# Optimization experiments

Measured on AMD Instinct MI355X. Metric: run time of the kernel, lower is better.

## Reference

```python
import jax, jax.numpy as jnp
import numpy as np

B, TQ, TS, E, D = 8, 100, 100, 512, 512

def setup_inputs() -> dict:
    key = jax.random.key(0)
    k1, k2, k3, k4, k5 = jax.random.split(key, 5)
    src_reps = jax.random.normal(k1, (B, TQ, TS, E), dtype=jnp.float32)
    tgt_reps = jax.random.normal(k2, (B, TQ, TS, E), dtype=jnp.float32)
    mask = jnp.ones((B, TQ, TS), dtype=jnp.float32)
    # attn_1: Linear(2E -> D) with bias; attn_2: Linear(D -> 1) no bias
    W1 = jax.random.normal(k3, (2 * E, D), dtype=jnp.float32) / np.sqrt(2 * E)
    b1 = jax.random.normal(k4, (D,), dtype=jnp.float32) * 0.01
    w2 = jax.random.normal(k5, (D,), dtype=jnp.float32) / np.sqrt(D)
    return {"src_reps": src_reps, "tgt_reps": tgt_reps, "mask": mask,
            "W1": W1, "b1": b1, "w2": w2}

def reference(src_reps, tgt_reps, mask, W1, b1, w2):
    # cat over feature dim: [B,TQ,TS,2E]
    cat_reps = jnp.concatenate([src_reps, tgt_reps], axis=-1)
    # two small linears + tanh -> scores [B,TQ,TS]
    h = jnp.tanh(jnp.einsum('bqse,ed->bqsd', cat_reps, W1) + b1)
    attn_scores = jnp.einsum('bqsd,d->bqs', h, w2)
    attn_scores = mask * attn_scores  # multiplicative mask (as in source)
    attn_weights = jax.nn.softmax(attn_scores, axis=2)
    # weighted sum over src dim -> [B,TQ,E]
    attn_out = jnp.einsum('bqs,bqse->bqe', attn_weights, src_reps)
    return (attn_out, attn_weights)
```

## Files before the change

kernel.cpp:

```cpp
#include <hip/hip_runtime.h>
#include <hip/hip_bf16.h>

#define B_   8
#define TQ_  100
#define TS_  100
#define E_   512
#define D_   512
#define K_   1024
#define M_   (B_*TQ_*TS_)

#define MT   128
#define NT   512
#define BK   64
#define NTHREADS 512

typedef __attribute__((ext_vector_type(4))) float f32x4;
typedef __attribute__((ext_vector_type(8))) short bf16x8;

__device__ __forceinline__ short f2bf(float f) {
  __hip_bfloat16 h = __float2bfloat16(f);
  return *reinterpret_cast<short*>(&h);
}

__device__ __forceinline__ float fast_tanh(float x) {
  float e = __expf(2.0f * x);
  return 1.0f - 2.0f / (e + 1.0f);
}

__device__ __forceinline__ void gld16(const void* g, void* l) {
  __builtin_amdgcn_global_load_lds(
      (const __attribute__((address_space(1))) unsigned int*)g,
      (__attribute__((address_space(3))) unsigned int*)l, 16, 0, 0);
}

__global__ void prep_w1(const float* __restrict__ W1, short* __restrict__ W1sw) {
  int idx = blockIdx.x * 256 + threadIdx.x;
  int k = idx >> 9;
  int n = idx & (D_ - 1);
  int byte = (k * 2) ^ ((n & 7) << 4);
  W1sw[(size_t)n * K_ + (byte >> 1)] = f2bf(W1[idx]);
}

__launch_bounds__(NTHREADS, 2)
__global__ void scores_kernel(const float* __restrict__ src,
                              const float* __restrict__ tgt,
                              const short* __restrict__ W1sw,
                              const float* __restrict__ b1,
                              const float* __restrict__ w2,
                              float* __restrict__ scores) {
  __shared__ __align__(16) char Alds[2][MT * 128];
  __shared__ __align__(16) char Blds[2][NT * 128];

  const int tid  = threadIdx.x;
  const int wave = tid >> 6;
  const int lane = tid & 63;
  const int lr   = lane & 15;
  const int lg   = lane >> 4;
  const int wr   = wave >> 2;
  const int wc   = wave & 3;
  const int m0   = blockIdx.x * MT;

  f32x4 acc[4][8];
  #pragma unroll
  for (int i = 0; i < 4; i++)
    #pragma unroll
    for (int j = 0; j < 8; j++)
      acc[i][j] = (f32x4){0.f, 0.f, 0.f, 0.f};

  const int ra  = tid >> 2;
  const int ka  = (tid & 3) * 16;
  const int swA = (ra & 7) << 4;
  const int br = tid >> 3;
  const int bb = (tid & 7) * 16;

  #define ISSUE_A(R0,R1,R2,R3,K0)                                              \
    {                                                                          \
      const float* Ap = (((K0) < E_) ? src : tgt)                              \
                        + (size_t)(m0 + ra) * E_ + ((K0) & (E_ - 1)) + ka;     \
      R0 = *reinterpret_cast<const f32x4*>(Ap);                                \
      R1 = *reinterpret_cast<const f32x4*>(Ap + 4);                            \
      R2 = *reinterpret_cast<const f32x4*>(Ap + 8);                            \
      R3 = *reinterpret_cast<const f32x4*>(Ap + 12);                           \
    }

  #define WRITE_A(R0,R1,R2,R3,BUF)                                             \
    {                                                                          \
      bf16x8 w0, w1;                                                           \
      w0[0]=f2bf(R0[0]); w0[1]=f2bf(R0[1]); w0[2]=f2bf(R0[2]); w0[3]=f2bf(R0[3]);\
      w0[4]=f2bf(R1[0]); w0[5]=f2bf(R1[1]); w0[6]=f2bf(R1[2]); w0[7]=f2bf(R1[3]);\
      w1[0]=f2bf(R2[0]); w1[1]=f2bf(R2[1]); w1[2]=f2bf(R2[2]); w1[3]=f2bf(R2[3]);\
      w1[4]=f2bf(R3[0]); w1[5]=f2bf(R3[1]); w1[6]=f2bf(R3[2]); w1[7]=f2bf(R3[3]);\
      int kb = ka * 2;                                                         \
      *reinterpret_cast<bf16x8*>((BUF) + ra * 128 + ( kb       ^ swA)) = w0;   \
      *reinterpret_cast<bf16x8*>((BUF) + ra * 128 + ((kb + 16) ^ swA)) = w1;   \
    }

  #define ISSUE_B(K0,BUF)                                                      \
    {                                                                          \
      _Pragma("unroll")                                                        \
      for (int j = 0; j < 8; j++) {                                            \
        const char* gp = (const char*)W1sw + (size_t)(j * 64 + br) * 2048      \
                         + (size_t)(K0) * 2 + bb;                              \
        gld16(gp, (BUF) + j * 8192 + tid * 16);                                \
      }                                                                        \
    }

  #define MFMA_PHASE(KK,AB,BB2)                                                \
    {                                                                          \
      const int kb = (KK) * 64 + lg * 16;                                      \
      bf16x8 a[4], b[8];                                                       \
      _Pragma("unroll")                                                        \
      for (int mi = 0; mi < 4; mi++) {                                         \
        int row = wr * 64 + mi * 16 + lr;                                      \
        a[mi] = *reinterpret_cast<const bf16x8*>(                              \
                    (AB) + row * 128 + (kb ^ ((row & 7) << 4)));               \
      }                                                                        \
      _Pragma("unroll")                                                        \
      for (int ni = 0; ni < 8; ni++) {                                         \
        int nr = wc * 128 + ni * 16 + lr;                                      \
        b[ni] = *reinterpret_cast<const bf16x8*>(                              \
                    (BB2) + nr * 128 + (kb ^ ((nr & 7) << 4)));                \
      }                                                                        \
      __builtin_amdgcn_s_setprio(1);                                           \
      _Pragma("unroll")                                                        \
      for (int mi = 0; mi < 4; mi++)                                           \
        _Pragma("unroll")                                                      \
        for (int ni = 0; ni < 8; ni++)                                         \
          acc[mi][ni] = __builtin_amdgcn_mfma_f32_16x16x32_bf16(               \
                            a[mi], b[ni], acc[mi][ni], 0, 0, 0);               \
      __builtin_amdgcn_s_setprio(0);                                           \
    }

  {
    f32x4 r0, r1, r2, r3;
    ISSUE_A(r0, r1, r2, r3, 0);
    ISSUE_B(0, Blds[0]);
    WRITE_A(r0, r1, r2, r3, Alds[0]);
  }
  __syncthreads();

  for (int t = 0; t < 16; ++t) {
    const int cur = t & 1;
    const int nxt = cur ^ 1;
    const bool pf = (t < 15);
    const int k0n = (t + 1) * BK;
    f32x4 r0, r1, r2, r3;
    if (pf) ISSUE_A(r0, r1, r2, r3, k0n);
    MFMA_PHASE(0, Alds[cur], Blds[cur]);
    if (pf) {
      ISSUE_B(k0n, Blds[nxt]);
      WRITE_A(r0, r1, r2, r3, Alds[nxt]);
    }
    MFMA_PHASE(1, Alds[cur], Blds[cur]);
    __syncthreads();
  }

  float* s_sc = (float*)Alds;
  if (tid < MT) s_sc[tid] = 0.0f;
  __syncthreads();

  float b1v[8], w2v[8];
  #pragma unroll
  for (int ni = 0; ni < 8; ni++) {
    int n = wc * 128 + ni * 16 + lr;
    b1v[ni] = b1[n];
    w2v[ni] = w2[n];
  }
  #pragma unroll
  for (int mi = 0; mi < 4; mi++) {
    #pragma unroll
    for (int r = 0; r < 4; r++) {
      float p = 0.0f;
      #pragma unroll
      for (int ni = 0; ni < 8; ni++)
        p += fast_tanh(acc[mi][ni][r] + b1v[ni]) * w2v[ni];
      p += __shfl_xor(p, 1);
      p += __shfl_xor(p, 2);
      p += __shfl_xor(p, 4);
      p += __shfl_xor(p, 8);
      if (lr == 0) atomicAdd(&s_sc[wr * 64 + mi * 16 + lg * 4 + r], p);
    }
  }
  __syncthreads();
  if (tid < MT) scores[m0 + tid] = s_sc[tid];
}

__global__ void softmax_wsum(const float* __restrict__ src,
                             const float* __restrict__ mask,
                             const float* __restrict__ scores,
                             float* __restrict__ out) {
  const int row = blockIdx.x;
  const int tid = threadIdx.x;
  __shared__ float s_e[TS_];

  float v = 0.0f;
  if (tid < TS_) {
    v = scores[row * TS_ + tid] * mask[row * TS_ + tid];
    s_e[tid] = v;
  }
  __syncthreads();
  float mx = -3.0e38f;
  for (int s = 0; s < TS_; s++) mx = fmaxf(mx, s_e[s]);
  __syncthreads();
  if (tid < TS_) s_e[tid] = __expf(v - mx);
  __syncthreads();
  float sum = 0.0f;
  for (int s = 0; s < TS_; s++) sum += s_e[s];
  const float inv = 1.0f / sum;

  float* out_attn = out;
  float* out_w    = out + (size_t)B_ * TQ_ * E_;
  if (tid < TS_) out_w[row * TS_ + tid] = s_e[tid] * inv;

  const float* sp = src + (size_t)row * TS_ * E_ + tid;
  float acc = 0.0f;
  #pragma unroll 4
  for (int s = 0; s < TS_; s++) acc = fmaf(s_e[s], sp[(size_t)s * E_], acc);
  out_attn[row * E_ + tid] = acc * inv;
}

extern "C" void kernel_launch(void* const* d_in, const int* in_sizes, int n_in,
                              void* d_out, int out_size, void* d_ws, size_t ws_size,
                              hipStream_t stream) {
  const float* src  = (const float*)d_in[0];
  const float* tgt  = (const float*)d_in[1];
  const float* mask = (const float*)d_in[2];
  const float* W1   = (const float*)d_in[3];
  const float* b1   = (const float*)d_in[4];
  const float* w2   = (const float*)d_in[5];

  short* W1sw   = (short*)d_ws;
  float* scores = (float*)((char*)d_ws + (size_t)D_ * K_ * 2);

  float* out = (float*)d_out;

  hipLaunchKernelGGL(prep_w1, dim3((K_ * D_) / 256), dim3(256), 0, stream, W1, W1sw);
  hipLaunchKernelGGL(scores_kernel, dim3(M_ / MT), dim3(NTHREADS), 0, stream,
                     src, tgt, W1sw, b1, w2, scores);
  hipLaunchKernelGGL(softmax_wsum, dim3(B_ * TQ_), dim3(512), 0, stream,
                     src, mask, scores, out);
}
```

Baseline: 187.2 us.

## Interleave GEMM K-loop into four barrier-separated phases with explicit waitcnts

Restructures the scores GEMM main loop into four sub-phases, each reading two B column tiles from LDS and issuing a slice of the next tile's global loads (A fp32 loads, B global_load_lds in halves, then the A bf16 write). Raw s_barrier and explicit s_waitcnt with sched_barrier replace __syncthreads, so memory traffic is spread between MFMA bursts instead of clustered. A fragments for both k halves are loaded once per tile. The cost is more barriers per iteration and fragile hand-tuned vmcnt counts.

```diff
diff --git a/kernel.cpp b/kernel.cpp
--- a/kernel.cpp
+++ b/kernel.cpp
@@ -9,8 +9,7 @@
 #define K_   1024
 #define M_   (B_*TQ_*TS_)
 
-#define MT   128
-#define NT   512
+#define BM   128
 #define BK   64
 #define NTHREADS 512
 
@@ -48,8 +47,8 @@
                               const float* __restrict__ b1,
                               const float* __restrict__ w2,
                               float* __restrict__ scores) {
-  __shared__ __align__(16) char Alds[2][MT * 128];
-  __shared__ __align__(16) char Blds[2][NT * 128];
+  __shared__ __align__(16) char Alds[2][BM * 128];
+  __shared__ __align__(16) char Blds[2][D_ * 128];
 
   const int tid  = threadIdx.x;
   const int wave = tid >> 6;
@@ -58,7 +57,7 @@
   const int lg   = lane >> 4;
   const int wr   = wave >> 2;
   const int wc   = wave & 3;
-  const int m0   = blockIdx.x * MT;
+  const int m0   = blockIdx.x * BM;
 
   f32x4 acc[4][8];
   #pragma unroll
@@ -68,95 +67,141 @@
       acc[i][j] = (f32x4){0.f, 0.f, 0.f, 0.f};
 
   const int ra  = tid >> 2;
-  const int ka  = (tid & 3) * 16;
-  const int swA = (ra & 7) << 4;
-  const int br = tid >> 3;
-  const int bb = (tid & 7) * 16;
-
-  #define ISSUE_A(R0,R1,R2,R3,K0)                                              \
-    {                                                                          \
-      const float* Ap = (((K0) < E_) ? src : tgt)                              \
-                        + (size_t)(m0 + ra) * E_ + ((K0) & (E_ - 1)) + ka;     \
-      R0 = *reinterpret_cast<const f32x4*>(Ap);                                \
-      R1 = *reinterpret_cast<const f32x4*>(Ap + 4);                            \
-      R2 = *reinterpret_cast<const f32x4*>(Ap + 8);                            \
-      R3 = *reinterpret_cast<const f32x4*>(Ap + 12);                           \
-    }
-
-  #define WRITE_A(R0,R1,R2,R3,BUF)                                             \
-    {                                                                          \
-      bf16x8 w0, w1;                                                           \
-      w0[0]=f2bf(R0[0]); w0[1]=f2bf(R0[1]); w0[2]=f2bf(R0[2]); w0[3]=f2bf(R0[3]);\
-      w0[4]=f2bf(R1[0]); w0[5]=f2bf(R1[1]); w0[6]=f2bf(R1[2]); w0[7]=f2bf(R1[3]);\
-      w1[0]=f2bf(R2[0]); w1[1]=f2bf(R2[1]); w1[2]=f2bf(R2[2]); w1[3]=f2bf(R2[3]);\
-      w1[4]=f2bf(R3[0]); w1[5]=f2bf(R3[1]); w1[6]=f2bf(R3[2]); w1[7]=f2bf(R3[3]);\
-      int kb = ka * 2;                                                         \
-      *reinterpret_cast<bf16x8*>((BUF) + ra * 128 + ( kb       ^ swA)) = w0;   \
-      *reinterpret_cast<bf16x8*>((BUF) + ra * 128 + ((kb + 16) ^ swA)) = w1;   \
-    }
-
-  #define ISSUE_B(K0,BUF)                                                      \
-    {                                                                          \
+  const int kaf = (tid & 3) * 16;
+  const int asw = (ra & 7) << 4;
+  const size_t arow = (size_t)(m0 + ra) * E_;
+  const size_t bgrow = (size_t)(tid >> 3) * 2048 + (size_t)(tid & 7) * 16;
+
+  #define WAIT_LGKM0  { asm volatile("s_waitcnt lgkmcnt(0)" ::: "memory"); \
+                        __builtin_amdgcn_sched_barrier(0); }
+  #define BAR         __builtin_amdgcn_s_barrier()
+
+  #define RD_B(BB, NI0, CUR)                                                   \
+    _Pragma("unroll")                                                          \
+    for (int u = 0; u < 2; u++) {                                              \
+      int n = wc * 128 + ((NI0) + u) * 16 + lr;                                \
       _Pragma("unroll")                                                        \
-      for (int j = 0; j < 8; j++) {                                            \
-        const char* gp = (const char*)W1sw + (size_t)(j * 64 + br) * 2048      \
-                         + (size_t)(K0) * 2 + bb;                              \
-        gld16(gp, (BUF) + j * 8192 + tid * 16);                                \
-      }                                                                        \
-    }
-
-  #define MFMA_PHASE(KK,AB,BB2)                                                \
-    {                                                                          \
-      const int kb = (KK) * 64 + lg * 16;                                      \
-      bf16x8 a[4], b[8];                                                       \
+      for (int kk = 0; kk < 2; kk++)                                           \
+        BB[u][kk] = *(const bf16x8*)(Blds[CUR] + n * 128 +                     \
+                        ((kk * 64 + lg * 16) ^ ((n & 7) << 4)));               \
+    }
+
+  #define MFMA8(BB, NI0)                                                       \
+    { __builtin_amdgcn_s_setprio(1);                                           \
       _Pragma("unroll")                                                        \
-      for (int mi = 0; mi < 4; mi++) {                                         \
-        int row = wr * 64 + mi * 16 + lr;                                      \
-        a[mi] = *reinterpret_cast<const bf16x8*>(                              \
-                    (AB) + row * 128 + (kb ^ ((row & 7) << 4)));               \
-      }                                                                        \
-      _Pragma("unroll")                                                        \
-      for (int ni = 0; ni < 8; ni++) {                                         \
-        int nr = wc * 128 + ni * 16 + lr;                                      \
-        b[ni] = *reinterpret_cast<const bf16x8*>(                              \
-                    (BB2) + nr * 128 + (kb ^ ((nr & 7) << 4)));                \
-      }                                                                        \
-      __builtin_amdgcn_s_setprio(1);                                           \
-      _Pragma("unroll")                                                        \
-      for (int mi = 0; mi < 4; mi++)                                           \
+      for (int kk = 0; kk < 2; kk++)                                           \
         _Pragma("unroll")                                                      \
-        for (int ni = 0; ni < 8; ni++)                                         \
-          acc[mi][ni] = __builtin_amdgcn_mfma_f32_16x16x32_bf16(               \
-                            a[mi], b[ni], acc[mi][ni], 0, 0, 0);               \
-      __builtin_amdgcn_s_setprio(0);                                           \
-    }
+        for (int mi = 0; mi < 4; mi++)                                         \
+          _Pragma("unroll")                                                    \
+          for (int u = 0; u < 2; u++)                                          \
+            acc[mi][(NI0) + u] = __builtin_amdgcn_mfma_f32_16x16x32_bf16(      \
+                a[mi][kk], BB[u][kk], acc[mi][(NI0) + u], 0, 0, 0);            \
+      __builtin_amdgcn_s_setprio(0); }
 
   {
-    f32x4 r0, r1, r2, r3;
-    ISSUE_A(r0, r1, r2, r3, 0);
-    ISSUE_B(0, Blds[0]);
-    WRITE_A(r0, r1, r2, r3, Alds[0]);
-  }
-  __syncthreads();
+    #pragma unroll
+    for (int j = 0; j < 8; j++)
+      gld16((const char*)W1sw + (size_t)j * 131072 + bgrow,
+            Blds[0] + j * 8192 + wave * 1024);
+    const float* Ap = src + arow + kaf;
+    f32x4 r0 = *(const f32x4*)(Ap);
+    f32x4 r1 = *(const f32x4*)(Ap + 4);
+    f32x4 r2 = *(const f32x4*)(Ap + 8);
+    f32x4 r3 = *(const f32x4*)(Ap + 12);
+    bf16x8 w0, w1;
+    w0[0]=f2bf(r0[0]); w0[1]=f2bf(r0[1]); w0[2]=f2bf(r0[2]); w0[3]=f2bf(r0[3]);
+    w0[4]=f2bf(r1[0]); w0[5]=f2bf(r1[1]); w0[6]=f2bf(r1[2]); w0[7]=f2bf(r1[3]);
+    w1[0]=f2bf(r2[0]); w1[1]=f2bf(r2[1]); w1[2]=f2bf(r2[2]); w1[3]=f2bf(r2[3]);
+    w1[4]=f2bf(r3[0]); w1[5]=f2bf(r3[1]); w1[6]=f2bf(r3[2]); w1[7]=f2bf(r3[3]);
+    int kb = kaf * 2;
+    *(bf16x8*)(Alds[0] + ra * 128 + ( kb       ^ asw)) = w0;
+    *(bf16x8*)(Alds[0] + ra * 128 + ((kb + 16) ^ asw)) = w1;
+    asm volatile("s_waitcnt vmcnt(0) lgkmcnt(0)" ::: "memory");
+    __builtin_amdgcn_sched_barrier(0);
+    BAR;
+  }
 
   for (int t = 0; t < 16; ++t) {
     const int cur = t & 1;
     const int nxt = cur ^ 1;
     const bool pf = (t < 15);
-    const int k0n = (t + 1) * BK;
+    const int kn  = (t + 1) * BK;
     f32x4 r0, r1, r2, r3;
-    if (pf) ISSUE_A(r0, r1, r2, r3, k0n);
-    MFMA_PHASE(0, Alds[cur], Blds[cur]);
-    if (pf) {
-      ISSUE_B(k0n, Blds[nxt]);
-      WRITE_A(r0, r1, r2, r3, Alds[nxt]);
-    }
-    MFMA_PHASE(1, Alds[cur], Blds[cur]);
-    __syncthreads();
+    bf16x8 a[4][2];
+
+    #pragma unroll
+    for (int mi = 0; mi < 4; mi++) {
+      int row = wr * 64 + mi * 16 + lr;
+      #pragma unroll
+      for (int kk = 0; kk < 2; kk++)
+        a[mi][kk] = *(const bf16x8*)(Alds[cur] + row * 128 +
+                        ((kk * 64 + lg * 16) ^ ((row & 7) << 4)));
+    }
+    {
+      bf16x8 bb[2][2];
+      RD_B(bb, 0, cur);
+      if (pf) {
+        const float* Ap = ((kn < E_) ? src : tgt) + arow + (kn & (E_ - 1)) + kaf;
+        r0 = *(const f32x4*)(Ap);
+        r1 = *(const f32x4*)(Ap + 4);
+        r2 = *(const f32x4*)(Ap + 8);
+        r3 = *(const f32x4*)(Ap + 12);
+      }
+      BAR; WAIT_LGKM0;
+      MFMA8(bb, 0);
+      BAR;
+    }
+    {
+      bf16x8 bb[2][2];
+      RD_B(bb, 2, cur);
+      if (pf) {
+        #pragma unroll
+        for (int j = 0; j < 4; j++)
+          gld16((const char*)W1sw + (size_t)j * 131072 + (size_t)kn * 2 + bgrow,
+                Blds[nxt] + j * 8192 + wave * 1024);
+      }
+      BAR; WAIT_LGKM0;
+      MFMA8(bb, 2);
+      BAR;
+    }
+    {
+      bf16x8 bb[2][2];
+      RD_B(bb, 4, cur);
+      if (pf) {
+        #pragma unroll
+        for (int j = 4; j < 8; j++)
+          gld16((const char*)W1sw + (size_t)j * 131072 + (size_t)kn * 2 + bgrow,
+                Blds[nxt] + j * 8192 + wave * 1024);
+      }
+      BAR; WAIT_LGKM0;
+      MFMA8(bb, 4);
+      BAR;
+    }
+    {
+      bf16x8 bb[2][2];
+      RD_B(bb, 6, cur);
+      if (pf) {
+        asm volatile("s_waitcnt vmcnt(8)" ::: "memory");
+        __builtin_amdgcn_sched_barrier(0);
+        bf16x8 w0, w1;
+        w0[0]=f2bf(r0[0]); w0[1]=f2bf(r0[1]); w0[2]=f2bf(r0[2]); w0[3]=f2bf(r0[3]);
+        w0[4]=f2bf(r1[0]); w0[5]=f2bf(r1[1]); w0[6]=f2bf(r1[2]); w0[7]=f2bf(r1[3]);
+        w1[0]=f2bf(r2[0]); w1[1]=f2bf(r2[1]); w1[2]=f2bf(r2[2]); w1[3]=f2bf(r2[3]);
+        w1[4]=f2bf(r3[0]); w1[5]=f2bf(r3[1]); w1[6]=f2bf(r3[2]); w1[7]=f2bf(r3[3]);
+        int kb = kaf * 2;
+        *(bf16x8*)(Alds[nxt] + ra * 128 + ( kb       ^ asw)) = w0;
+        *(bf16x8*)(Alds[nxt] + ra * 128 + ((kb + 16) ^ asw)) = w1;
+      }
+      BAR; WAIT_LGKM0;
+      MFMA8(bb, 6);
+      asm volatile("s_waitcnt vmcnt(0) lgkmcnt(0)" ::: "memory");
+      __builtin_amdgcn_sched_barrier(0);
+      BAR;
+    }
   }
 
   float* s_sc = (float*)Alds;
-  if (tid < MT) s_sc[tid] = 0.0f;
+  if (tid < BM) s_sc[tid] = 0.0f;
   __syncthreads();
 
   float b1v[8], w2v[8];
@@ -182,7 +227,7 @@
     }
   }
   __syncthreads();
-  if (tid < MT) scores[m0 + tid] = s_sc[tid];
+  if (tid < BM) scores[m0 + tid] = s_sc[tid];
 }
 
 __global__ void softmax_wsum(const float* __restrict__ src,
@@ -235,7 +280,7 @@
   float* out = (float*)d_out;
 
   hipLaunchKernelGGL(prep_w1, dim3((K_ * D_) / 256), dim3(256), 0, stream, W1, W1sw);
-  hipLaunchKernelGGL(scores_kernel, dim3(M_ / MT), dim3(NTHREADS), 0, stream,
+  hipLaunchKernelGGL(scores_kernel, dim3(M_ / BM), dim3(NTHREADS), 0, stream,
                      src, tgt, W1sw, b1, w2, scores);
   hipLaunchKernelGGL(softmax_wsum, dim3(B_ * TQ_), dim3(512), 0, stream,
                      src, mask, scores, out);
```

Measured after the change: 185.2 us. About the same (-1.1%).

## Hand-schedule GEMM main loop with explicit waitcnts and sched barriers

Applied to the files above, without the earlier changes.

Restructures the scores GEMM loop so both A and B prefetches for the next K tile are issued at the top of the iteration. All A fragments for the tile are loaded once, and the conversion and LDS write of A are deferred until after the MFMAs, gated by explicit vmcnt/lgkmcnt waits and sched_barriers. __syncthreads is replaced with raw s_barrier. The aim is better overlap of global loads with MFMA work and less compiler-inserted waiting. The cost is fragile manual counter management and more live registers for the A fragments.

```diff
diff --git a/kernel.cpp b/kernel.cpp
--- a/kernel.cpp
+++ b/kernel.cpp
@@ -9,8 +9,7 @@
 #define K_   1024
 #define M_   (B_*TQ_*TS_)
 
-#define MT   128
-#define NT   512
+#define BM   128
 #define BK   64
 #define NTHREADS 512
 
@@ -48,8 +47,8 @@
                               const float* __restrict__ b1,
                               const float* __restrict__ w2,
                               float* __restrict__ scores) {
-  __shared__ __align__(16) char Alds[2][MT * 128];
-  __shared__ __align__(16) char Blds[2][NT * 128];
+  __shared__ __align__(16) char Alds[2][BM * 128];
+  __shared__ __align__(16) char Blds[2][D_ * 128];
 
   const int tid  = threadIdx.x;
   const int wave = tid >> 6;
@@ -58,7 +57,7 @@
   const int lg   = lane >> 4;
   const int wr   = wave >> 2;
   const int wc   = wave & 3;
-  const int m0   = blockIdx.x * MT;
+  const int m0   = blockIdx.x * BM;
 
   f32x4 acc[4][8];
   #pragma unroll
@@ -68,95 +67,97 @@
       acc[i][j] = (f32x4){0.f, 0.f, 0.f, 0.f};
 
   const int ra  = tid >> 2;
-  const int ka  = (tid & 3) * 16;
-  const int swA = (ra & 7) << 4;
-  const int br = tid >> 3;
-  const int bb = (tid & 7) * 16;
-
-  #define ISSUE_A(R0,R1,R2,R3,K0)                                              \
-    {                                                                          \
-      const float* Ap = (((K0) < E_) ? src : tgt)                              \
-                        + (size_t)(m0 + ra) * E_ + ((K0) & (E_ - 1)) + ka;     \
-      R0 = *reinterpret_cast<const f32x4*>(Ap);                                \
-      R1 = *reinterpret_cast<const f32x4*>(Ap + 4);                            \
-      R2 = *reinterpret_cast<const f32x4*>(Ap + 8);                            \
-      R3 = *reinterpret_cast<const f32x4*>(Ap + 12);                           \
-    }
-
-  #define WRITE_A(R0,R1,R2,R3,BUF)                                             \
-    {                                                                          \
-      bf16x8 w0, w1;                                                           \
-      w0[0]=f2bf(R0[0]); w0[1]=f2bf(R0[1]); w0[2]=f2bf(R0[2]); w0[3]=f2bf(R0[3]);\
-      w0[4]=f2bf(R1[0]); w0[5]=f2bf(R1[1]); w0[6]=f2bf(R1[2]); w0[7]=f2bf(R1[3]);\
-      w1[0]=f2bf(R2[0]); w1[1]=f2bf(R2[1]); w1[2]=f2bf(R2[2]); w1[3]=f2bf(R2[3]);\
-      w1[4]=f2bf(R3[0]); w1[5]=f2bf(R3[1]); w1[6]=f2bf(R3[2]); w1[7]=f2bf(R3[3]);\
-      int kb = ka * 2;                                                         \
-      *reinterpret_cast<bf16x8*>((BUF) + ra * 128 + ( kb       ^ swA)) = w0;   \
-      *reinterpret_cast<bf16x8*>((BUF) + ra * 128 + ((kb + 16) ^ swA)) = w1;   \
-    }
-
-  #define ISSUE_B(K0,BUF)                                                      \
-    {                                                                          \
-      _Pragma("unroll")                                                        \
-      for (int j = 0; j < 8; j++) {                                            \
-        const char* gp = (const char*)W1sw + (size_t)(j * 64 + br) * 2048      \
-                         + (size_t)(K0) * 2 + bb;                              \
-        gld16(gp, (BUF) + j * 8192 + tid * 16);                                \
-      }                                                                        \
-    }
-
-  #define MFMA_PHASE(KK,AB,BB2)                                                \
-    {                                                                          \
-      const int kb = (KK) * 64 + lg * 16;                                      \
-      bf16x8 a[4], b[8];                                                       \
-      _Pragma("unroll")                                                        \
-      for (int mi = 0; mi < 4; mi++) {                                         \
-        int row = wr * 64 + mi * 16 + lr;                                      \
-        a[mi] = *reinterpret_cast<const bf16x8*>(                              \
-                    (AB) + row * 128 + (kb ^ ((row & 7) << 4)));               \
-      }                                                                        \
+  const int kaf = (tid & 3) * 16;
+  const int asw = (ra & 7) << 4;
+  const size_t arow = (size_t)(m0 + ra) * E_;
+  const size_t bgrow = (size_t)(tid >> 3) * 2048 + (size_t)(tid & 7) * 16;
+
+  #define SBAR0       __builtin_amdgcn_sched_barrier(0)
+  #define WAIT_LGKM0  { asm volatile("s_waitcnt lgkmcnt(0)" ::: "memory"); SBAR0; }
+
+  #define ISSUE_A(K0)                                                          \
+    { const float* Ap = (((K0) < E_) ? src : tgt) + arow + ((K0) & (E_-1)) + kaf; \
+      r0 = *(const f32x4*)(Ap);                                                \
+      r1 = *(const f32x4*)(Ap + 4);                                            \
+      r2 = *(const f32x4*)(Ap + 8);                                            \
+      r3 = *(const f32x4*)(Ap + 12); }
+
+  #define ISSUE_B(K0, NX)                                                      \
+    { _Pragma("unroll")                                                        \
+      for (int j = 0; j < 8; j++)                                              \
+        gld16((const char*)W1sw + (size_t)j * 131072 + (size_t)(K0) * 2 + bgrow, \
+              Blds[NX] + j * 8192 + wave * 1024); }
+
+  #define WRITE_A(NX)                                                          \
+    { bf16x8 w0, w1;                                                           \
+      w0[0]=f2bf(r0[0]); w0[1]=f2bf(r0[1]); w0[2]=f2bf(r0[2]); w0[3]=f2bf(r0[3]); \
+      w0[4]=f2bf(r1[0]); w0[5]=f2bf(r1[1]); w0[6]=f2bf(r1[2]); w0[7]=f2bf(r1[3]); \
+      w1[0]=f2bf(r2[0]); w1[1]=f2bf(r2[1]); w1[2]=f2bf(r2[2]); w1[3]=f2bf(r2[3]); \
+      w1[4]=f2bf(r3[0]); w1[5]=f2bf(r3[1]); w1[6]=f2bf(r3[2]); w1[7]=f2bf(r3[3]); \
+      int kb = kaf * 2;                                                        \
+      *(bf16x8*)(Alds[NX] + ra * 128 + ( kb       ^ asw)) = w0;                \
+      *(bf16x8*)(Alds[NX] + ra * 128 + ((kb + 16) ^ asw)) = w1; }
+
+  #define HALF_K(KK, CUR)                                                      \
+    { bf16x8 b[8];                                                             \
       _Pragma("unroll")                                                        \
       for (int ni = 0; ni < 8; ni++) {                                         \
-        int nr = wc * 128 + ni * 16 + lr;                                      \
-        b[ni] = *reinterpret_cast<const bf16x8*>(                              \
-                    (BB2) + nr * 128 + (kb ^ ((nr & 7) << 4)));                \
+        int n = wc * 128 + ni * 16 + lr;                                       \
+        b[ni] = *(const bf16x8*)(Blds[CUR] + n * 128 +                         \
+                    (((KK) * 64 + lg * 16) ^ ((n & 7) << 4)));                 \
       }                                                                        \
+      WAIT_LGKM0;                                                              \
       __builtin_amdgcn_s_setprio(1);                                           \
       _Pragma("unroll")                                                        \
       for (int mi = 0; mi < 4; mi++)                                           \
         _Pragma("unroll")                                                      \
         for (int ni = 0; ni < 8; ni++)                                         \
           acc[mi][ni] = __builtin_amdgcn_mfma_f32_16x16x32_bf16(               \
-                            a[mi], b[ni], acc[mi][ni], 0, 0, 0);               \
-      __builtin_amdgcn_s_setprio(0);                                           \
-    }
-
-  {
-    f32x4 r0, r1, r2, r3;
-    ISSUE_A(r0, r1, r2, r3, 0);
-    ISSUE_B(0, Blds[0]);
-    WRITE_A(r0, r1, r2, r3, Alds[0]);
-  }
-  __syncthreads();
+              a[mi][KK], b[ni], acc[mi][ni], 0, 0, 0);                         \
+      __builtin_amdgcn_s_setprio(0); }
+
+  f32x4 r0, r1, r2, r3;
+
+  ISSUE_A(0); SBAR0;
+  ISSUE_B(0, 0); SBAR0;
+  asm volatile("s_waitcnt vmcnt(8)" ::: "memory"); SBAR0;
+  WRITE_A(0);
+  asm volatile("s_waitcnt vmcnt(0) lgkmcnt(0)" ::: "memory"); SBAR0;
+  __builtin_amdgcn_s_barrier();
 
   for (int t = 0; t < 16; ++t) {
     const int cur = t & 1;
     const int nxt = cur ^ 1;
     const bool pf = (t < 15);
-    const int k0n = (t + 1) * BK;
-    f32x4 r0, r1, r2, r3;
-    if (pf) ISSUE_A(r0, r1, r2, r3, k0n);
-    MFMA_PHASE(0, Alds[cur], Blds[cur]);
+    const int kn  = (t + 1) * BK;
+
     if (pf) {
-      ISSUE_B(k0n, Blds[nxt]);
-      WRITE_A(r0, r1, r2, r3, Alds[nxt]);
-    }
-    MFMA_PHASE(1, Alds[cur], Blds[cur]);
-    __syncthreads();
+      ISSUE_A(kn); SBAR0;
+      ISSUE_B(kn, nxt); SBAR0;
+    }
+
+    bf16x8 a[4][2];
+    #pragma unroll
+    for (int mi = 0; mi < 4; mi++) {
+      int row = wr * 64 + mi * 16 + lr;
+      #pragma unroll
+      for (int kk = 0; kk < 2; kk++)
+        a[mi][kk] = *(const bf16x8*)(Alds[cur] + row * 128 +
+                        ((kk * 64 + lg * 16) ^ ((row & 7) << 4)));
+    }
+    HALF_K(0, cur);
+    HALF_K(1, cur);
+
+    if (pf) {
+      asm volatile("s_waitcnt vmcnt(8)" ::: "memory"); SBAR0;
+      WRITE_A(nxt);
+      asm volatile("s_waitcnt vmcnt(0) lgkmcnt(0)" ::: "memory"); SBAR0;
+    }
+    __builtin_amdgcn_s_barrier();
   }
 
   float* s_sc = (float*)Alds;
-  if (tid < MT) s_sc[tid] = 0.0f;
+  if (tid < BM) s_sc[tid] = 0.0f;
   __syncthreads();
 
   float b1v[8], w2v[8];
@@ -182,7 +183,7 @@
     }
   }
   __syncthreads();
-  if (tid < MT) scores[m0 + tid] = s_sc[tid];
+  if (tid < BM) scores[m0 + tid] = s_sc[tid];
 }
 
 __global__ void softmax_wsum(const float* __restrict__ src,
@@ -235,7 +236,7 @@
   float* out = (float*)d_out;
 
   hipLaunchKernelGGL(prep_w1, dim3((K_ * D_) / 256), dim3(256), 0, stream, W1, W1sw);
-  hipLaunchKernelGGL(scores_kernel, dim3(M_ / MT), dim3(NTHREADS), 0, stream,
+  hipLaunchKernelGGL(scores_kernel, dim3(M_ / BM), dim3(NTHREADS), 0, stream,
                      src, tgt, W1sw, b1, w2, scores);
   hipLaunchKernelGGL(softmax_wsum, dim3(B_ * TQ_), dim3(512), 0, stream,
                      src, mask, scores, out);
```

Result: no change. 190.8 us (+1.9%).
